# Kernel tuning notes

Measured on AMD Instinct MI355X. Metric: run time of the kernel, lower is better.

The kernel has to match this reference:

```python
import jax, jax.numpy as jnp
import numpy as np

N = 100000       # nodes
E = 1600000      # edges
F_IN = 128       # num_features
DIM = 128        # hidden dim
L = 3            # num_gc_layers
G = 512          # num graphs
EPS = 1e-5       # BatchNorm eps


def setup_inputs() -> dict:
    key = jax.random.key(0)
    ks = jax.random.split(key, 3 + 4 * L)
    d = {
        "x": jax.random.normal(ks[0], (N, F_IN), jnp.float32),
        "edge_index": jax.random.randint(ks[1], (2, E), 0, N, dtype=jnp.int32).astype(jnp.int64),
        "batch": jnp.sort(jax.random.randint(ks[2], (N,), 0, G, dtype=jnp.int32)).astype(jnp.int64),
    }
    fin = F_IN
    for i in range(L):
        d[f"W{i}"] = jax.random.normal(ks[3 + 4 * i], (fin, DIM), jnp.float32) / np.float32(np.sqrt(fin))
        d[f"b{i}"] = jnp.zeros((DIM,), jnp.float32)
        d[f"g{i}"] = jnp.ones((DIM,), jnp.float32)   # BN gamma
        d[f"t{i}"] = jnp.zeros((DIM,), jnp.float32)  # BN beta
        fin = DIM
    return d


def _gcn_layer(h, src, dst, norm, W, b):
    # GCNConv: (xW) gathered at src, degree-normalized, scatter-added at dst, + bias
    h = h @ W                                    # [N, DIM] small GEMM
    msg = h[src] * norm[:, None]                 # [E+N, DIM] gather (memory-bound)
    out = jax.ops.segment_sum(msg, dst, num_segments=N)
    return out + b


def _forward(x, edge_index, batch, params):
    loops = jnp.arange(N, dtype=edge_index.dtype)
    src = jnp.concatenate([edge_index[0], loops])   # add self-loops (PyG default)
    dst = jnp.concatenate([edge_index[1], loops])
    deg = jax.ops.segment_sum(jnp.ones_like(src, jnp.float32), dst, num_segments=N)
    dinv = jax.lax.rsqrt(jnp.maximum(deg, 1.0))     # deg >= 1 due to self-loops
    norm = dinv[src] * dinv[dst]

    pools = []
    h = x
    for (W, b, g, t) in params:
        h = jax.nn.relu(_gcn_layer(h, src, dst, norm, W, b))
        # BatchNorm1d (training-mode batch stats, biased variance)
        mu = h.mean(axis=0)
        var = h.var(axis=0)
        h = (h - mu) * jax.lax.rsqrt(var + EPS) * g + t
        # global_add_pool per layer
        pools.append(jax.ops.segment_sum(h, batch, num_segments=G))
    return jnp.concatenate(pools, axis=1)  # [G, L*DIM]


def reference(x, edge_index, batch, W0, b0, g0, t0, W1, b1, g1, t1, W2, b2, g2, t2):
    params = [(W0, b0, g0, t0), (W1, b1, g1, t1), (W2, b2, g2, t2)]
    return _forward(x, edge_index, batch, params)
```

## Files before the change

### kernel.cpp

```cpp
#include <hip/hip_runtime.h>

#define NNODES 100000
#define NEDGES 1600000
#define NGRAPH 512
#define EPSBN 1e-5f
#define DEGCAP 64
#define NBUCK 512
#define BSH 8
#define BCAP 4864
#define P1_BLOCKS ((NEDGES + 4095)/4096)
#define GEMM_BLOCKS ((NNODES + 63)/64)

typedef unsigned short ushort_t;
typedef unsigned int uint_t;

typedef __attribute__((ext_vector_type(8))) __bf16 bf16x8;
typedef __attribute__((ext_vector_type(4))) float f32x4;
typedef __attribute__((ext_vector_type(2))) uint_t uintx2;

__device__ __forceinline__ float b2f(ushort_t u){ return __uint_as_float(((uint_t)u)<<16); }
__device__ __forceinline__ ushort_t f2b(float f){
  union { __bf16 h; ushort_t u; } c;
  c.h = (__bf16)f;
  return c.u;
}
__device__ __forceinline__ uint_t pkbf(float a, float b){
  union { __bf16 h[2]; uint_t u; } c;
  c.h[0] = (__bf16)a; c.h[1] = (__bf16)b;
  return c.u;
}
__device__ __forceinline__ float lo16(uint_t d){ return b2f((ushort_t)(d & 0xffffu)); }
__device__ __forceinline__ float hi16(uint_t d){ return b2f((ushort_t)(d >> 16)); }

__device__ __forceinline__ f32x4 mfma_bf16(bf16x8 a, bf16x8 b, f32x4 c){
  return __builtin_amdgcn_mfma_f32_16x16x32_bf16(a, b, c, 0, 0, 0);
}

union Frag8 { ushort_t u[8]; bf16x8 v; };

__device__ __forceinline__ bf16x8 cvt8_f32_bf16(const float* __restrict__ p){
  float4 v0 = *(const float4*)(const void*)p;
  float4 v1 = *(const float4*)(const void*)(p + 4);
  Frag8 f;
  f.u[0] = f2b(v0.x); f.u[1] = f2b(v0.y); f.u[2] = f2b(v0.z); f.u[3] = f2b(v0.w);
  f.u[4] = f2b(v1.x); f.u[5] = f2b(v1.y); f.u[6] = f2b(v1.z); f.u[7] = f2b(v1.w);
  return f.v;
}

__global__ __launch_bounds__(256) void k_p1(const int* __restrict__ src,
                                            const int* __restrict__ dst,
                                            int* __restrict__ gBucket,
                                            int2* __restrict__ ebuf,
                                            const int* __restrict__ batch,
                                            int* __restrict__ gstart,
                                            const float* __restrict__ x,
                                            const float* __restrict__ W0,
                                            ushort_t* __restrict__ hs){
  __shared__ __attribute__((aligned(16))) ushort_t sMem[128*136];

  if (blockIdx.x < P1_BLOCKS){
    int* cntL  = (int*)sMem;
    int* baseL = cntL + NBUCK;
    int* ofsL  = baseL + NBUCK;
    int t = threadIdx.x;
    #pragma unroll
    for (int r = 0; r < 2; ++r){
      int i = t + r*256;
      cntL[i] = 0; ofsL[i] = 0;
    }
    __syncthreads();

    int base = blockIdx.x * 4096;
    int e0 = base + t*16;
    int s[16], d[16];
    int ne = 0;
    if (e0 + 16 <= NEDGES){
      #pragma unroll
      for (int q = 0; q < 4; ++q){
        int4 sv = *(const int4*)(src + e0 + q*4);
        int4 dv = *(const int4*)(dst + e0 + q*4);
        s[q*4+0]=sv.x; s[q*4+1]=sv.y; s[q*4+2]=sv.z; s[q*4+3]=sv.w;
        d[q*4+0]=dv.x; d[q*4+1]=dv.y; d[q*4+2]=dv.z; d[q*4+3]=dv.w;
      }
      ne = 16;
    } else {
      for (int e = e0; e < NEDGES && ne < 16; ++e, ++ne){
        s[ne] = src[e]; d[ne] = dst[e];
      }
    }
    for (int k = 0; k < ne; ++k) atomicAdd(&cntL[d[k] >> BSH], 1);
    __syncthreads();
    #pragma unroll
    for (int r = 0; r < 2; ++r){
      int i = t + r*256;
      int c = cntL[i];
      baseL[i] = c ? atomicAdd(&gBucket[i*16], c) : 0;
    }
    __syncthreads();
    for (int k = 0; k < ne; ++k){
      int b = d[k] >> BSH;
      int o = atomicAdd(&ofsL[b], 1);
      ebuf[(size_t)b*BCAP + baseL[b] + o] = make_int2(s[k], d[k]);
    }
    return;
  }
  if (blockIdx.x == P1_BLOCKS){
    #pragma unroll
    for (int r = 0; r < 2; ++r){
      int g = threadIdx.x + r*256;
      int lo = 0, hi = NNODES;
      while (lo < hi){
        int mid = (lo + hi) >> 1;
        if (batch[mid] < g) lo = mid + 1; else hi = mid;
      }
      gstart[g] = lo;
    }
    if (threadIdx.x == 0) gstart[NGRAPH] = NNODES;
    return;
  }

  ushort_t* sWT = sMem;
  int bb = blockIdx.x - P1_BLOCKS - 1;
  for (int idx = threadIdx.x; idx < 128*128; idx += 256){
    int c = idx >> 7, jj = idx & 127;
    sWT[jj*136 + c] = f2b(W0[idx]);
  }
  __syncthreads();

  int wave = threadIdx.x >> 6;
  int lane = threadIdx.x & 63;
  int quad = lane >> 4;
  int l16  = lane & 15;
  int row0 = bb*64 + wave*16;

  int m  = row0 + l16;
  int mc = (m < NNODES) ? m : (NNODES - 1);

  const float* ap = x + (size_t)mc*128 + quad*8;
  bf16x8 af0 = cvt8_f32_bf16(ap);
  bf16x8 af1 = cvt8_f32_bf16(ap + 32);
  bf16x8 af2 = cvt8_f32_bf16(ap + 64);
  bf16x8 af3 = cvt8_f32_bf16(ap + 96);

  f32x4 acc[8];
  #pragma unroll
  for (int ct = 0; ct < 8; ++ct){
    const ushort_t* bp = sWT + (ct*16 + l16)*136 + quad*8;
    bf16x8 b0 = *(const bf16x8*)(const void*)(bp);
    bf16x8 b1 = *(const bf16x8*)(const void*)(bp + 32);
    bf16x8 b2 = *(const bf16x8*)(const void*)(bp + 64);
    bf16x8 b3 = *(const bf16x8*)(const void*)(bp + 96);
    f32x4 a_ = {0.f, 0.f, 0.f, 0.f};
    a_ = mfma_bf16(af0, b0, a_);
    a_ = mfma_bf16(af1, b1, a_);
    a_ = mfma_bf16(af2, b2, a_);
    a_ = mfma_bf16(af3, b3, a_);
    acc[ct] = a_;
  }

  int rbase = row0 + quad*4;
  #pragma unroll
  for (int ct = 0; ct < 8; ++ct){
    int colc = ct*16 + l16;
    #pragma unroll
    for (int rg = 0; rg < 4; ++rg){
      int rr = rbase + rg;
      if (rr < NNODES) hs[(size_t)rr*128 + colc] = f2b(acc[ct][rg]);
    }
  }
}

__global__ __launch_bounds__(256) void k_p2(const int2* __restrict__ ebuf,
                                            const int* __restrict__ gBucket,
                                            int* __restrict__ colx,
                                            int* __restrict__ cnt){
  __shared__ int slotcnt[256];
  int t = threadIdx.x;
  int b = blockIdx.x;
  slotcnt[t] = 0;
  __syncthreads();

  int nb = gBucket[b*16];
  int vbase = b << BSH;

  for (int e = t; e < nb; e += 256){
    int2 p = ebuf[(size_t)b*BCAP + e];
    int slot = atomicAdd(&slotcnt[p.y - vbase], 1);
    colx[p.y*DEGCAP + slot] = p.x;
  }
  __syncthreads();

  int v = vbase + t;
  if (v < NNODES){
    int c = slotcnt[t];
    cnt[v] = c;
    int ce = (c <= 15) ? 15 : 31;
    for (int s = c; s < ce; ++s) colx[(size_t)v*DEGCAP + s] = NNODES;
  }
}

#define NORM_BLOCKS 1024
__global__ __launch_bounds__(256) void k_norm(const int* __restrict__ cnt,
                                              ushort_t* __restrict__ hs){
  uintx2* H2 = (uintx2*)hs;
  const int total = NNODES*32;
  for (int i = blockIdx.x*256 + threadIdx.x; i < total; i += NORM_BLOCKS*256){
    int v = i >> 5;
    float dv = rsqrtf((float)(cnt[v] + 1));
    uintx2 d = H2[i];
    d.x = pkbf(lo16(d.x)*dv, hi16(d.x)*dv);
    d.y = pkbf(lo16(d.y)*dv, hi16(d.y)*dv);
    H2[i] = d;
  }
}

__global__ __launch_bounds__(256) void k_gemm(const ushort_t* __restrict__ A,
                                              const ushort_t* __restrict__ WT,
                                              const float* __restrict__ Kv,
                                              const int* __restrict__ cnt,
                                              ushort_t* __restrict__ hs){
  __shared__ __attribute__((aligned(16))) ushort_t sWT[128*136];
  {
    const uint4* sp = (const uint4*)WT;
    uint4* dp = (uint4*)sWT;
    for (int i = threadIdx.x; i < (128*136*2)/16; i += 256) dp[i] = sp[i];
  }
  __syncthreads();

  int wave = threadIdx.x >> 6;
  int lane = threadIdx.x & 63;
  int quad = lane >> 4;
  int l16  = lane & 15;
  int row0 = blockIdx.x*64 + wave*16;

  int m  = row0 + l16;
  int mc = (m < NNODES) ? m : (NNODES - 1);

  const ushort_t* ap = A + (size_t)mc*128 + quad*8;
  bf16x8 af0 = *(const bf16x8*)(const void*)(ap);
  bf16x8 af1 = *(const bf16x8*)(const void*)(ap + 32);
  bf16x8 af2 = *(const bf16x8*)(const void*)(ap + 64);
  bf16x8 af3 = *(const bf16x8*)(const void*)(ap + 96);

  f32x4 acc[8];
  #pragma unroll
  for (int ct = 0; ct < 8; ++ct){
    const ushort_t* bp = sWT + (ct*16 + l16)*136 + quad*8;
    bf16x8 b0 = *(const bf16x8*)(const void*)(bp);
    bf16x8 b1 = *(const bf16x8*)(const void*)(bp + 32);
    bf16x8 b2 = *(const bf16x8*)(const void*)(bp + 64);
    bf16x8 b3 = *(const bf16x8*)(const void*)(bp + 96);
    f32x4 a_ = {0.f, 0.f, 0.f, 0.f};
    a_ = mfma_bf16(af0, b0, a_);
    a_ = mfma_bf16(af1, b1, a_);
    a_ = mfma_bf16(af2, b2, a_);
    a_ = mfma_bf16(af3, b3, a_);
    acc[ct] = a_;
  }

  int rbase = row0 + quad*4;
  float dv[4];
  #pragma unroll
  for (int rg = 0; rg < 4; ++rg){
    int rr = rbase + rg;
    int cc = cnt[(rr < NNODES) ? rr : (NNODES - 1)];
    dv[rg] = rsqrtf((float)(cc + 1));
  }
  #pragma unroll
  for (int ct = 0; ct < 8; ++ct){
    int colc = ct*16 + l16;
    float kv = Kv[colc];
    #pragma unroll
    for (int rg = 0; rg < 4; ++rg){
      int rr = rbase + rg;
      if (rr < NNODES){
        float val = (acc[ct][rg] + kv) * dv[rg];
        hs[(size_t)rr*128 + colc] = f2b(val);
      }
    }
  }
}

#define AGG_BLOCKS 1024
#define AGG_WAVES (AGG_BLOCKS*4)
#define AGG_CHUNK ((NNODES + AGG_WAVES - 1) / AGG_WAVES)

#define FENCE8(A) asm volatile("" :: \
  "v"(A[0]),"v"(A[1]),"v"(A[2]),"v"(A[3]),"v"(A[4]),"v"(A[5]),"v"(A[6]),"v"(A[7]))

#define ISSUE_R0(dst, cr, vv) do { \
  _Pragma("unroll") \
  for (int k_ = 0; k_ < 8; ++k_){ \
    int uA_ = (k_ == 0) ? (vv) : __builtin_amdgcn_readlane((cr), 2*k_ - 1); \
    int uB_ = __builtin_amdgcn_readlane((cr), 2*k_); \
    int u_  = sel ? uB_ : uA_; \
    (dst)[k_] = H2[(uint_t)u_*32u + m]; \
  } \
} while(0)

#define ISSUE_R1(dst, cr) do { \
  _Pragma("unroll") \
  for (int k_ = 0; k_ < 8; ++k_){ \
    int uA_ = __builtin_amdgcn_readlane((cr), 15 + 2*k_); \
    int uB_ = __builtin_amdgcn_readlane((cr), 16 + 2*k_); \
    int u_  = sel ? uB_ : uA_; \
    (dst)[k_] = H2[(uint_t)u_*32u + m]; \
  } \
} while(0)

#define CONSUME8(A) do { \
  FENCE8(A); \
  _Pragma("unroll") \
  for (int k_ = 0; k_ < 8; ++k_){ \
    a0 += lo16((A)[k_].x); a1 += hi16((A)[k_].x); \
    a2 += lo16((A)[k_].y); a3 += hi16((A)[k_].y); \
  } \
} while(0)

template<bool WR>
__global__ __launch_bounds__(256, 4) void k_agg(const ushort_t* __restrict__ hs,
                                                const int* __restrict__ cnt,
                                                const int* __restrict__ colx,
                                                const float* __restrict__ bias,
                                                const int* __restrict__ batch,
                                                ushort_t* __restrict__ rout,
                                                float* __restrict__ poolS,
                                                float* __restrict__ chansum,
                                                float* __restrict__ chansumsq){
  __shared__ float bsum[128];
  __shared__ float bsq[128];
  if (threadIdx.x < 128){ bsum[threadIdx.x] = 0.f; bsq[threadIdx.x] = 0.f; }
  __syncthreads();

  int wave = __builtin_amdgcn_readfirstlane((blockIdx.x << 2) + (threadIdx.x >> 6));
  int lane = threadIdx.x & 63;
  int m    = lane & 31;
  int sel  = lane >> 5;
  int n0 = wave * AGG_CHUNK;
  int n1 = (n0 + AGG_CHUNK < NNODES) ? (n0 + AGG_CHUNK) : NNODES;

  const uintx2* H2 = (const uintx2*)hs;
  uintx2* R2 = (uintx2*)rout;

  float bbv[4];
  #pragma unroll
  for (int i = 0; i < 4; ++i) bbv[i] = bias[4*m + i];
  int chbase = 4*m + 2*sel;

  float ss0 = 0.f, ss1 = 0.f, sq0 = 0.f, sq1 = 0.f;
  float p0 = 0.f, p1 = 0.f;
  int curg = -1;

  if (n0 < n1){
    int cr0 = colx[(size_t)n0*DEGCAP + lane];
    int cv0 = cnt[n0];
    int cr1 = 0, cv1 = 0;
    if (n0 + 1 < n1){
      cr1 = colx[(size_t)(n0+1)*DEGCAP + lane];
      cv1 = cnt[n0+1];
    }
    uintx2 e0[8], e1[8];
    ISSUE_R0(e0, cr0, n0);
    if (cv0 > 15) ISSUE_R1(e1, cr0);
    else { _Pragma("unroll") for (int k_ = 0; k_ < 8; ++k_) e1[k_] = (uintx2){0u,0u}; }

    for (int v = n0; v < n1; ++v){
      int v2 = v + 2;
      int cr2 = 0, cv2 = 0;
      if (v2 < n1){
        cr2 = colx[(size_t)v2*DEGCAP + lane];
        cv2 = cnt[v2];
      }

      uintx2 f0[8], f1[8];
      bool hasn = (v + 1 < n1);
      if (hasn){
        ISSUE_R0(f0, cr1, v + 1);
        if (cv1 > 15) ISSUE_R1(f1, cr1);
        else { _Pragma("unroll") for (int k_ = 0; k_ < 8; ++k_) f1[k_] = (uintx2){0u,0u}; }
      } else {
        _Pragma("unroll") for (int k_ = 0; k_ < 8; ++k_){ f0[k_] = (uintx2){0u,0u}; f1[k_] = (uintx2){0u,0u}; }
      }

      int g = batch[v];
      if (g != curg){
        if (curg >= 0){
          atomicAdd(&poolS[curg*128 + chbase],     p0);
          atomicAdd(&poolS[curg*128 + chbase + 1], p1);
        }
        p0 = 0.f; p1 = 0.f; curg = g;
      }

      float a0 = 0.f, a1 = 0.f, a2 = 0.f, a3 = 0.f;

      CONSUME8(e0);
      if (cv0 > 15) CONSUME8(e1);
      if (cv0 > 31){
        for (int j = 31; j < cv0; j += 2){
          int uA = __builtin_amdgcn_readlane(cr0, j);
          int uB = (j + 1 < cv0) ? __builtin_amdgcn_readlane(cr0, j + 1) : NNODES;
          int u  = sel ? uB : uA;
          uintx2 dd = H2[(uint_t)u*32u + m];
          a0 += lo16(dd.x); a1 += hi16(dd.x);
          a2 += lo16(dd.y); a3 += hi16(dd.y);
        }
      }

      float s0 = a0 + __shfl_xor(a0, 32, 64);
      float s1 = a1 + __shfl_xor(a1, 32, 64);
      float s2 = a2 + __shfl_xor(a2, 32, 64);
      float s3 = a3 + __shfl_xor(a3, 32, 64);

      float dvv = rsqrtf((float)(cv0 + 1));
      float r0 = fmaxf(s0*dvv + bbv[0], 0.f);
      float r1 = fmaxf(s1*dvv + bbv[1], 0.f);
      float r2 = fmaxf(s2*dvv + bbv[2], 0.f);
      float r3 = fmaxf(s3*dvv + bbv[3], 0.f);
      if constexpr (WR){
        if (lane < 32){
          uintx2 wv;
          wv.x = pkbf(r0, r1);
          wv.y = pkbf(r2, r3);
          R2[(uint_t)v*32u + m] = wv;
        }
      }
      float cA = sel ? r2 : r0;
      float cB = sel ? r3 : r1;
      ss0 += cA; ss1 += cB;
      sq0 += cA*cA; sq1 += cB*cB;
      p0 += cA; p1 += cB;

      cr0 = cr1; cv0 = cv1;
      cr1 = cr2; cv1 = cv2;
      #pragma unroll
      for (int k_ = 0; k_ < 8; ++k_){ e0[k_] = f0[k_]; e1[k_] = f1[k_]; }
    }
  }

  if (curg >= 0){
    atomicAdd(&poolS[curg*128 + chbase],     p0);
    atomicAdd(&poolS[curg*128 + chbase + 1], p1);
  }
  atomicAdd(&bsum[chbase],     ss0);
  atomicAdd(&bsum[chbase + 1], ss1);
  atomicAdd(&bsq[chbase],      sq0);
  atomicAdd(&bsq[chbase + 1],  sq1);
  __syncthreads();
  if (threadIdx.x < 128){
    atomicAdd(&chansum[threadIdx.x],   bsum[threadIdx.x]);
    atomicAdd(&chansumsq[threadIdx.x], bsq[threadIdx.x]);
  }
}

__global__ void k_fold(const float* __restrict__ Wn,
                       const float* __restrict__ chansum, const float* __restrict__ chansumsq,
                       const float* __restrict__ gamma, const float* __restrict__ beta,
                       ushort_t* __restrict__ WT, float* __restrict__ Kv,
                       float* __restrict__ avec, float* __restrict__ cvec){
  __shared__ float red[128];
  int j = blockIdx.x, c = threadIdx.x;
  const float invN = 1.0f / (float)NNODES;
  float mu  = chansum[c] * invN;
  float var = chansumsq[c] * invN - mu*mu;
  float a = gamma[c] * rsqrtf(var + EPSBN);
  float cc = beta[c] - mu*a;
  if (j == 0){ avec[c] = a; cvec[c] = cc; }
  float wv = Wn[c*128 + j];
  WT[j*136 + c] = f2b(a * wv);
  red[c] = cc * wv;
  __syncthreads();
  for (int off = 64; off > 0; off >>= 1){
    if (c < off) red[c] += red[c + off];
    __syncthreads();
  }
  if (c == 0) Kv[j] = red[0];
}

__global__ void k_final(const float* __restrict__ poolS, const int* __restrict__ gstart,
                        const float* __restrict__ avec, const float* __restrict__ cvec,
                        const float* __restrict__ chansum2, const float* __restrict__ chansumsq2,
                        const float* __restrict__ gamma2, const float* __restrict__ beta2,
                        float* __restrict__ out){
  int g = blockIdx.x, c = threadIdx.x;
  float n = (float)(gstart[g + 1] - gstart[g]);
  #pragma unroll
  for (int i = 0; i < 2; ++i){
    float v = avec[i*128 + c] * poolS[((size_t)i*NGRAPH + g)*128 + c] + n * cvec[i*128 + c];
    out[(size_t)g*384 + i*128 + c] = v;
  }
  const float invN = 1.0f / (float)NNODES;
  float mu  = chansum2[c] * invN;
  float var = chansumsq2[c] * invN - mu*mu;
  float a2 = gamma2[c] * rsqrtf(var + EPSBN);
  float c2 = beta2[c] - mu*a2;
  float v2 = a2 * poolS[((size_t)2*NGRAPH + g)*128 + c] + n * c2;
  out[(size_t)g*384 + 2*128 + c] = v2;
}

extern "C" void kernel_launch(void* const* d_in, const int* in_sizes, int n_in,
                              void* d_out, int out_size, void* d_ws, size_t ws_size,
                              hipStream_t stream){
  (void)in_sizes; (void)n_in; (void)out_size; (void)ws_size;

  const float* x     = (const float*)d_in[0];
  const int*   ei    = (const int*)d_in[1];
  const int*   batch = (const int*)d_in[2];
  const float* Wp[3] = {(const float*)d_in[3], (const float*)d_in[7],  (const float*)d_in[11]};
  const float* bp[3] = {(const float*)d_in[4], (const float*)d_in[8],  (const float*)d_in[12]};
  const float* gp[3] = {(const float*)d_in[5], (const float*)d_in[9],  (const float*)d_in[13]};
  const float* tp[3] = {(const float*)d_in[6], (const float*)d_in[10], (const float*)d_in[14]};
  const int* srcp = ei;
  const int* dstp = ei + NEDGES;

  char* w = (char*)d_ws;
  size_t off = 0;
  auto take = [&](size_t bytes) -> char* {
    char* p = w + off;
    off += (bytes + 511) & ~(size_t)511;
    return p;
  };
  int*      cnt       = (int*)take((size_t)NNODES*4);
  int*      colx      = (int*)take((size_t)NNODES*DEGCAP*4);
  int*      gstart    = (int*)take((NGRAPH+1)*4);
  ushort_t* hs        = (ushort_t*)take((size_t)(NNODES+1)*128*2);
  ushort_t* rbuf      = (ushort_t*)take((size_t)NNODES*128*2);
  ushort_t* WT        = (ushort_t*)take(128*136*2);
  float*    Kv        = (float*)take(128*4);
  float*    chanstats = (float*)take(3*256*4);
  float*    poolS     = (float*)take((size_t)3*NGRAPH*128*4);
  float*    avec      = (float*)take(2*128*4);
  float*    cvec      = (float*)take(2*128*4);
  int*      gBucket   = (int*)take(NBUCK*16*4);

  int2* ebuf = (int2*)rbuf;

  hipMemsetAsync(gBucket,   0, NBUCK*16*4,             stream);
  hipMemsetAsync(poolS,     0, (size_t)3*NGRAPH*128*4, stream);
  hipMemsetAsync(chanstats, 0, 3*256*4,                stream);
  hipMemsetAsync(hs + (size_t)NNODES*128, 0, 128*2,    stream);

  k_p1<<<P1_BLOCKS + 1 + GEMM_BLOCKS, 256, 0, stream>>>(
      srcp, dstp, gBucket, ebuf, batch, gstart, x, Wp[0], hs);
  k_p2<<<NBUCK, 256, 0, stream>>>(ebuf, gBucket, colx, cnt);
  k_norm<<<NORM_BLOCKS, 256, 0, stream>>>(cnt, hs);

  k_agg<true><<<AGG_BLOCKS, 256, 0, stream>>>(hs, cnt, colx, bp[0], batch, rbuf,
                                              poolS, chanstats, chanstats + 128);
  k_fold<<<128, 128, 0, stream>>>(Wp[1], chanstats, chanstats + 128,
                                  gp[0], tp[0], WT, Kv, avec, cvec);
  k_gemm<<<GEMM_BLOCKS, 256, 0, stream>>>(rbuf, WT, Kv, cnt, hs);
  k_agg<true><<<AGG_BLOCKS, 256, 0, stream>>>(hs, cnt, colx, bp[1], batch, rbuf,
                                              poolS + (size_t)NGRAPH*128,
                                              chanstats + 256, chanstats + 256 + 128);
  k_fold<<<128, 128, 0, stream>>>(Wp[2], chanstats + 256, chanstats + 256 + 128,
                                  gp[1], tp[1], WT, Kv, avec + 128, cvec + 128);
  k_gemm<<<GEMM_BLOCKS, 256, 0, stream>>>(rbuf, WT, Kv, cnt, hs);
  k_agg<false><<<AGG_BLOCKS, 256, 0, stream>>>(hs, cnt, colx, bp[2], batch, rbuf,
                                               poolS + (size_t)2*NGRAPH*128,
                                               chanstats + 512, chanstats + 512 + 128);

  k_final<<<NGRAPH, 128, 0, stream>>>(poolS, gstart, avec, cvec,
                                      chanstats + 512, chanstats + 512 + 128,
                                      gp[2], tp[2], (float*)d_out);
}
```

Baseline: 442.8 us.

## Slice node features into 16-channel column panels and restructure aggregation per slice

The bf16 feature buffers change from row-major [N,128] to eight column slices of [N+1,16]. Aggregation becomes one pass per slice, so each gather reads a 32-byte row that should stay cache-resident within a slice. Aggregation blocks now own contiguous node ranges, stage their neighbor lists in LDS, use 4 lanes per node with 16 nodes per wave, and pre-reduce pool sums in LDS for up to four graphs. In exchange, the old readlane-based two-node software pipeline is dropped, waves run a number of rounds set by the largest degree among their nodes, and the GEMM and normalization kernels gain strided slice accesses.

```diff
diff --git a/kernel.cpp b/kernel.cpp
--- a/kernel.cpp
+++ b/kernel.cpp
@@ -11,6 +11,9 @@
 #define P1_BLOCKS ((NEDGES + 4095)/4096)
 #define GEMM_BLOCKS ((NNODES + 63)/64)
 
+#define SROWS (NNODES + 1)
+#define SLICE_SH ((size_t)SROWS * 16)
+
 typedef unsigned short ushort_t;
 typedef unsigned int uint_t;
 
@@ -31,6 +34,10 @@
 }
 __device__ __forceinline__ float lo16(uint_t d){ return b2f((ushort_t)(d & 0xffffu)); }
 __device__ __forceinline__ float hi16(uint_t d){ return b2f((ushort_t)(d >> 16)); }
+
+__device__ __forceinline__ size_t hoff(int v, int c){
+  return (size_t)(c >> 4) * SLICE_SH + (size_t)v * 16 + (c & 15);
+}
 
 __device__ __forceinline__ f32x4 mfma_bf16(bf16x8 a, bf16x8 b, f32x4 c){
   return __builtin_amdgcn_mfma_f32_16x16x32_bf16(a, b, c, 0, 0, 0);
@@ -165,7 +172,7 @@
     #pragma unroll
     for (int rg = 0; rg < 4; ++rg){
       int rr = rbase + rg;
-      if (rr < NNODES) hs[(size_t)rr*128 + colc] = f2b(acc[ct][rg]);
+      if (rr < NNODES) hs[hoff(rr, colc)] = f2b(acc[ct][rg]);
     }
   }
 }
@@ -203,14 +210,17 @@
 __global__ __launch_bounds__(256) void k_norm(const int* __restrict__ cnt,
                                               ushort_t* __restrict__ hs){
   uintx2* H2 = (uintx2*)hs;
-  const int total = NNODES*32;
-  for (int i = blockIdx.x*256 + threadIdx.x; i < total; i += NORM_BLOCKS*256){
-    int v = i >> 5;
+  const size_t SL4 = (size_t)SROWS * 4;
+  for (int j = blockIdx.x*256 + threadIdx.x; j < NNODES*4; j += NORM_BLOCKS*256){
+    int v = j >> 2;
     float dv = rsqrtf((float)(cnt[v] + 1));
-    uintx2 d = H2[i];
-    d.x = pkbf(lo16(d.x)*dv, hi16(d.x)*dv);
-    d.y = pkbf(lo16(d.y)*dv, hi16(d.y)*dv);
-    H2[i] = d;
+    #pragma unroll
+    for (int s = 0; s < 8; ++s){
+      uintx2 d = H2[(size_t)s*SL4 + j];
+      d.x = pkbf(lo16(d.x)*dv, hi16(d.x)*dv);
+      d.y = pkbf(lo16(d.y)*dv, hi16(d.y)*dv);
+      H2[(size_t)s*SL4 + j] = d;
+    }
   }
 }
 
@@ -236,11 +246,11 @@
   int m  = row0 + l16;
   int mc = (m < NNODES) ? m : (NNODES - 1);
 
-  const ushort_t* ap = A + (size_t)mc*128 + quad*8;
-  bf16x8 af0 = *(const bf16x8*)(const void*)(ap);
-  bf16x8 af1 = *(const bf16x8*)(const void*)(ap + 32);
-  bf16x8 af2 = *(const bf16x8*)(const void*)(ap + 64);
-  bf16x8 af3 = *(const bf16x8*)(const void*)(ap + 96);
+  int c0 = quad*8;
+  bf16x8 af0 = *(const bf16x8*)(const void*)(A + hoff(mc, c0));
+  bf16x8 af1 = *(const bf16x8*)(const void*)(A + hoff(mc, c0 + 32));
+  bf16x8 af2 = *(const bf16x8*)(const void*)(A + hoff(mc, c0 + 64));
+  bf16x8 af3 = *(const bf16x8*)(const void*)(A + hoff(mc, c0 + 96));
 
   f32x4 acc[8];
   #pragma unroll
@@ -275,47 +285,18 @@
       int rr = rbase + rg;
       if (rr < NNODES){
         float val = (acc[ct][rg] + kv) * dv[rg];
-        hs[(size_t)rr*128 + colc] = f2b(val);
+        hs[hoff(rr, colc)] = f2b(val);
       }
     }
   }
 }
 
 #define AGG_BLOCKS 1024
-#define AGG_WAVES (AGG_BLOCKS*4)
-#define AGG_CHUNK ((NNODES + AGG_WAVES - 1) / AGG_WAVES)
+#define NPB 98
+#define NHEX 7
 
 #define FENCE8(A) asm volatile("" :: \
   "v"(A[0]),"v"(A[1]),"v"(A[2]),"v"(A[3]),"v"(A[4]),"v"(A[5]),"v"(A[6]),"v"(A[7]))
-
-#define ISSUE_R0(dst, cr, vv) do { \
-  _Pragma("unroll") \
-  for (int k_ = 0; k_ < 8; ++k_){ \
-    int uA_ = (k_ == 0) ? (vv) : __builtin_amdgcn_readlane((cr), 2*k_ - 1); \
-    int uB_ = __builtin_amdgcn_readlane((cr), 2*k_); \
-    int u_  = sel ? uB_ : uA_; \
-    (dst)[k_] = H2[(uint_t)u_*32u + m]; \
-  } \
-} while(0)
-
-#define ISSUE_R1(dst, cr) do { \
-  _Pragma("unroll") \
-  for (int k_ = 0; k_ < 8; ++k_){ \
-    int uA_ = __builtin_amdgcn_readlane((cr), 15 + 2*k_); \
-    int uB_ = __builtin_amdgcn_readlane((cr), 16 + 2*k_); \
-    int u_  = sel ? uB_ : uA_; \
-    (dst)[k_] = H2[(uint_t)u_*32u + m]; \
-  } \
-} while(0)
-
-#define CONSUME8(A) do { \
-  FENCE8(A); \
-  _Pragma("unroll") \
-  for (int k_ = 0; k_ < 8; ++k_){ \
-    a0 += lo16((A)[k_].x); a1 += hi16((A)[k_].x); \
-    a2 += lo16((A)[k_].y); a3 += hi16((A)[k_].y); \
-  } \
-} while(0)
 
 template<bool WR>
 __global__ __launch_bounds__(256, 4) void k_agg(const ushort_t* __restrict__ hs,
@@ -327,128 +308,133 @@
                                                 float* __restrict__ poolS,
                                                 float* __restrict__ chansum,
                                                 float* __restrict__ chansumsq){
+  __shared__ int colx_s[NPB*65];
   __shared__ float bsum[128];
   __shared__ float bsq[128];
-  if (threadIdx.x < 128){ bsum[threadIdx.x] = 0.f; bsq[threadIdx.x] = 0.f; }
-  __syncthreads();
-
-  int wave = __builtin_amdgcn_readfirstlane((blockIdx.x << 2) + (threadIdx.x >> 6));
-  int lane = threadIdx.x & 63;
-  int m    = lane & 31;
-  int sel  = lane >> 5;
-  int n0 = wave * AGG_CHUNK;
-  int n1 = (n0 + AGG_CHUNK < NNODES) ? (n0 + AGG_CHUNK) : NNODES;
+  __shared__ float poolL[4*128];
+
+  int tid = threadIdx.x;
+  if (tid < 128){ bsum[tid] = 0.f; bsq[tid] = 0.f; }
+  #pragma unroll
+  for (int r = 0; r < 2; ++r) poolL[tid + r*256] = 0.f;
+
+  int bn0 = blockIdx.x * NPB;
+  int rn = NNODES - bn0;
+  if (rn > NPB) rn = NPB;
+  if (rn < 0) rn = 0;
+
+  for (int i = tid; i < rn*64; i += 256){
+    int ln = i >> 6, sl = i & 63;
+    colx_s[ln*65 + sl] = colx[(size_t)(bn0 + ln)*64 + sl];
+  }
+  int gbase = (rn > 0) ? batch[bn0] : 0;
+  __syncthreads();
+
+  int wave = tid >> 6;
+  int lane = tid & 63;
+  int grp = lane >> 2;
+  int sub = lane & 3;
 
   const uintx2* H2 = (const uintx2*)hs;
   uintx2* R2 = (uintx2*)rout;
 
-  float bbv[4];
-  #pragma unroll
-  for (int i = 0; i < 4; ++i) bbv[i] = bias[4*m + i];
-  int chbase = 4*m + 2*sel;
-
-  float ss0 = 0.f, ss1 = 0.f, sq0 = 0.f, sq1 = 0.f;
-  float p0 = 0.f, p1 = 0.f;
-  int curg = -1;
-
-  if (n0 < n1){
-    int cr0 = colx[(size_t)n0*DEGCAP + lane];
-    int cv0 = cnt[n0];
-    int cr1 = 0, cv1 = 0;
-    if (n0 + 1 < n1){
-      cr1 = colx[(size_t)(n0+1)*DEGCAP + lane];
-      cv1 = cnt[n0+1];
-    }
-    uintx2 e0[8], e1[8];
-    ISSUE_R0(e0, cr0, n0);
-    if (cv0 > 15) ISSUE_R1(e1, cr0);
-    else { _Pragma("unroll") for (int k_ = 0; k_ < 8; ++k_) e1[k_] = (uintx2){0u,0u}; }
-
-    for (int v = n0; v < n1; ++v){
-      int v2 = v + 2;
-      int cr2 = 0, cv2 = 0;
-      if (v2 < n1){
-        cr2 = colx[(size_t)v2*DEGCAP + lane];
-        cv2 = cnt[v2];
-      }
-
-      uintx2 f0[8], f1[8];
-      bool hasn = (v + 1 < n1);
-      if (hasn){
-        ISSUE_R0(f0, cr1, v + 1);
-        if (cv1 > 15) ISSUE_R1(f1, cr1);
-        else { _Pragma("unroll") for (int k_ = 0; k_ < 8; ++k_) f1[k_] = (uintx2){0u,0u}; }
-      } else {
-        _Pragma("unroll") for (int k_ = 0; k_ < 8; ++k_){ f0[k_] = (uintx2){0u,0u}; f1[k_] = (uintx2){0u,0u}; }
-      }
-
-      int g = batch[v];
-      if (g != curg){
-        if (curg >= 0){
-          atomicAdd(&poolS[curg*128 + chbase],     p0);
-          atomicAdd(&poolS[curg*128 + chbase + 1], p1);
+  for (int s = 0; s < 8; ++s){
+    const uintx2* Hs = H2 + (size_t)s*SROWS*4;
+    uintx2* Rs = R2 + (size_t)s*SROWS*4;
+    float4 bb = *(const float4*)(bias + s*16 + sub*4);
+    float ss0=0.f, ss1=0.f, ss2=0.f, ss3=0.f;
+    float q0=0.f, q1=0.f, q2=0.f, q3=0.f;
+
+    for (int hx = wave; hx < NHEX; hx += 4){
+      if (hx*16 >= rn) break;
+      int ln = hx*16 + grp;
+      bool valid = (ln < rn);
+      int vg = bn0 + ln;
+      int cv = 0, g = 0;
+      if (valid){ cv = cnt[vg]; g = batch[vg]; }
+
+      int mx = cv;
+      mx = max(mx, __shfl_xor(mx, 4, 64));
+      mx = max(mx, __shfl_xor(mx, 8, 64));
+      mx = max(mx, __shfl_xor(mx, 16, 64));
+      mx = max(mx, __shfl_xor(mx, 32, 64));
+      int rounds = mx + 1;
+
+      int lnc = (ln < NPB) ? ln : (NPB - 1);
+      int lofs = lnc*65;
+      float a0=0.f, a1=0.f, a2=0.f, a3=0.f;
+
+      for (int rb = 0; rb < rounds; rb += 8){
+        uintx2 gb[8];
+        #pragma unroll
+        for (int k = 0; k < 8; ++k){
+          int r = rb + k;
+          int sl = r - 1; if (sl < 0) sl = 0;
+          int ui = colx_s[lofs + sl];
+          int u = (r == 0) ? (valid ? vg : NNODES)
+                           : ((r - 1 < cv) ? ui : NNODES);
+          gb[k] = Hs[(size_t)u*4 + sub];
         }
-        p0 = 0.f; p1 = 0.f; curg = g;
-      }
-
-      float a0 = 0.f, a1 = 0.f, a2 = 0.f, a3 = 0.f;
-
-      CONSUME8(e0);
-      if (cv0 > 15) CONSUME8(e1);
-      if (cv0 > 31){
-        for (int j = 31; j < cv0; j += 2){
-          int uA = __builtin_amdgcn_readlane(cr0, j);
-          int uB = (j + 1 < cv0) ? __builtin_amdgcn_readlane(cr0, j + 1) : NNODES;
-          int u  = sel ? uB : uA;
-          uintx2 dd = H2[(uint_t)u*32u + m];
-          a0 += lo16(dd.x); a1 += hi16(dd.x);
-          a2 += lo16(dd.y); a3 += hi16(dd.y);
+        FENCE8(gb);
+        #pragma unroll
+        for (int k = 0; k < 8; ++k){
+          a0 += lo16(gb[k].x); a1 += hi16(gb[k].x);
+          a2 += lo16(gb[k].y); a3 += hi16(gb[k].y);
         }
       }
 
-      float s0 = a0 + __shfl_xor(a0, 32, 64);
-      float s1 = a1 + __shfl_xor(a1, 32, 64);
-      float s2 = a2 + __shfl_xor(a2, 32, 64);
-      float s3 = a3 + __shfl_xor(a3, 32, 64);
-
-      float dvv = rsqrtf((float)(cv0 + 1));
-      float r0 = fmaxf(s0*dvv + bbv[0], 0.f);
-      float r1 = fmaxf(s1*dvv + bbv[1], 0.f);
-      float r2 = fmaxf(s2*dvv + bbv[2], 0.f);
-      float r3 = fmaxf(s3*dvv + bbv[3], 0.f);
-      if constexpr (WR){
-        if (lane < 32){
+      float dvv = rsqrtf((float)(cv + 1));
+      float r0 = fmaxf(a0*dvv + bb.x, 0.f);
+      float r1 = fmaxf(a1*dvv + bb.y, 0.f);
+      float r2 = fmaxf(a2*dvv + bb.z, 0.f);
+      float r3 = fmaxf(a3*dvv + bb.w, 0.f);
+
+      if (valid){
+        if constexpr (WR){
           uintx2 wv;
           wv.x = pkbf(r0, r1);
           wv.y = pkbf(r2, r3);
-          R2[(uint_t)v*32u + m] = wv;
+          Rs[(size_t)vg*4 + sub] = wv;
+        }
+        ss0 += r0; ss1 += r1; ss2 += r2; ss3 += r3;
+        q0 += r0*r0; q1 += r1*r1; q2 += r2*r2; q3 += r3*r3;
+        int cb = s*16 + sub*4;
+        int gs = g - gbase;
+        if (gs >= 0 && gs < 4){
+          atomicAdd(&poolL[gs*128 + cb + 0], r0);
+          atomicAdd(&poolL[gs*128 + cb + 1], r1);
+          atomicAdd(&poolL[gs*128 + cb + 2], r2);
+          atomicAdd(&poolL[gs*128 + cb + 3], r3);
+        } else {
+          atomicAdd(&poolS[(size_t)g*128 + cb + 0], r0);
+          atomicAdd(&poolS[(size_t)g*128 + cb + 1], r1);
+          atomicAdd(&poolS[(size_t)g*128 + cb + 2], r2);
+          atomicAdd(&poolS[(size_t)g*128 + cb + 3], r3);
         }
       }
-      float cA = sel ? r2 : r0;
-      float cB = sel ? r3 : r1;
-      ss0 += cA; ss1 += cB;
-      sq0 += cA*cA; sq1 += cB*cB;
-      p0 += cA; p1 += cB;
-
-      cr0 = cr1; cv0 = cv1;
-      cr1 = cr2; cv1 = cv2;
-      #pragma unroll
-      for (int k_ = 0; k_ < 8; ++k_){ e0[k_] = f0[k_]; e1[k_] = f1[k_]; }
-    }
-  }
-
-  if (curg >= 0){
-    atomicAdd(&poolS[curg*128 + chbase],     p0);
-    atomicAdd(&poolS[curg*128 + chbase + 1], p1);
-  }
-  atomicAdd(&bsum[chbase],     ss0);
-  atomicAdd(&bsum[chbase + 1], ss1);
-  atomicAdd(&bsq[chbase],      sq0);
-  atomicAdd(&bsq[chbase + 1],  sq1);
-  __syncthreads();
-  if (threadIdx.x < 128){
-    atomicAdd(&chansum[threadIdx.x],   bsum[threadIdx.x]);
-    atomicAdd(&chansumsq[threadIdx.x], bsq[threadIdx.x]);
+    }
+
+    int cb = s*16 + sub*4;
+    atomicAdd(&bsum[cb + 0], ss0);
+    atomicAdd(&bsum[cb + 1], ss1);
+    atomicAdd(&bsum[cb + 2], ss2);
+    atomicAdd(&bsum[cb + 3], ss3);
+    atomicAdd(&bsq[cb + 0], q0);
+    atomicAdd(&bsq[cb + 1], q1);
+    atomicAdd(&bsq[cb + 2], q2);
+    atomicAdd(&bsq[cb + 3], q3);
+  }
+
+  __syncthreads();
+  if (tid < 128){
+    atomicAdd(&chansum[tid],   bsum[tid]);
+    atomicAdd(&chansumsq[tid], bsq[tid]);
+  }
+  for (int i = tid; i < 512; i += 256){
+    int gs = i >> 7, c = i & 127;
+    float v = poolL[i];
+    int g = gbase + gs;
+    if (v != 0.f && g < NGRAPH) atomicAdd(&poolS[(size_t)g*128 + c], v);
   }
 }
 
@@ -522,8 +508,8 @@
   int*      cnt       = (int*)take((size_t)NNODES*4);
   int*      colx      = (int*)take((size_t)NNODES*DEGCAP*4);
   int*      gstart    = (int*)take((NGRAPH+1)*4);
-  ushort_t* hs        = (ushort_t*)take((size_t)(NNODES+1)*128*2);
-  ushort_t* rbuf      = (ushort_t*)take((size_t)NNODES*128*2);
+  ushort_t* hs        = (ushort_t*)take((size_t)SROWS*128*2);
+  ushort_t* rbuf      = (ushort_t*)take((size_t)SROWS*128*2);
   ushort_t* WT        = (ushort_t*)take(128*136*2);
   float*    Kv        = (float*)take(128*4);
   float*    chanstats = (float*)take(3*256*4);
@@ -537,7 +523,8 @@
   hipMemsetAsync(gBucket,   0, NBUCK*16*4,             stream);
   hipMemsetAsync(poolS,     0, (size_t)3*NGRAPH*128*4, stream);
   hipMemsetAsync(chanstats, 0, 3*256*4,                stream);
-  hipMemsetAsync(hs + (size_t)NNODES*128, 0, 128*2,    stream);
+  for (int s = 0; s < 8; ++s)
+    hipMemsetAsync(hs + (size_t)s*SLICE_SH + (size_t)NNODES*16, 0, 32, stream);
 
   k_p1<<<P1_BLOCKS + 1 + GEMM_BLOCKS, 256, 0, stream>>>(
       srcp, dstp, gBucket, ebuf, batch, gstart, x, Wp[0], hs);
```

Measured after the change: 846.4 us. 1.91x slower.
